# Optimization experiments

Hardware: AMD Instinct MI355X
Metric: run time of the kernel (lower is better)

The kernel has to match this reference:

```python
import jax, jax.numpy as jnp
import numpy as np

N, L, S, D, K, H, G = 512, 1024, 3, 128, 4, 32, 64


def setup_inputs() -> dict:
    key = jax.random.key(0)
    ks = jax.random.split(key, 12)
    f = lambda i, shape, s=1.0: jax.random.normal(ks[i], shape, dtype=jnp.float32) * s
    return dict(
        scores=f(0, (N, 1, L, S)),
        veh_repr=f(1, (N, 1, D)),
        cust_repr=f(2, (N, L, D)),
        edge_emb=f(3, (N, 1, L, D)),
        expert_w1=f(4, (K, S, H), 0.3),
        expert_b1=jnp.zeros((K, H), jnp.float32),
        expert_w2=f(5, (K, H, 1), 0.3),
        expert_b2=jnp.zeros((K, 1), jnp.float32),
        sit_w1=f(6, (2 * D, G), 0.05),
        sit_b1=jnp.zeros((G,), jnp.float32),
        sit_w2=f(7, (G, K), 0.1),
        sit_b2=jnp.zeros((K,), jnp.float32),
        cand_w=f(8, (S, K), 0.3),
        cand_b=jnp.zeros((K,), jnp.float32),
        edge_w=f(9, (D, K), 0.05),
        gate_balance=jnp.zeros((), jnp.float32),
    )


def reference(scores, veh_repr, cust_repr, edge_emb,
              expert_w1, expert_b1, expert_w2, expert_b2,
              sit_w1, sit_b1, sit_w2, sit_b2,
              cand_w, cand_b, edge_w, gate_balance):
    # Inference mode: no gate noise, no dropout (identity at eval).
    # Situation gating: vehicle repr + graph context -> (N,1,K) logits
    graph_ctx = cust_repr.mean(axis=1, keepdims=True)              # (N,1,D)
    sit_in = jnp.concatenate([veh_repr, graph_ctx], axis=-1)       # (N,1,2D)
    hg = jax.nn.gelu(sit_in @ sit_w1 + sit_b1, approximate=False)  # (N,1,G)
    sit_logits = hg @ sit_w2 + sit_b2                              # (N,1,K)

    # Candidate-level gating from raw scores + edge embeddings
    cand_logits = scores @ cand_w + cand_b + edge_emb @ edge_w     # (N,1,L,K)

    alpha = jax.nn.sigmoid(gate_balance)
    gate_logits = alpha * sit_logits[:, :, None, :] + (1.0 - alpha) * cand_logits
    gate_w = jax.nn.softmax(gate_logits, axis=-1)                  # (N,1,L,K)

    # Per-expert tiny MLP over the S score channels
    h = jax.nn.gelu(jnp.einsum('nqls,ksh->nqlkh', scores, expert_w1) + expert_b1,
                    approximate=False)                             # (N,1,L,K,H)
    expert_out = jnp.einsum('nqlkh,kho->nqlko', h, expert_w2)[..., 0] + expert_b2[:, 0]

    fused = (gate_w * expert_out).sum(axis=-1)                     # (N,1,L)
    return fused
```

## Files before the change

kernel.cpp:

```cpp
#include <hip/hip_runtime.h>

#define NN 512
#define LL 1024
#define SS 3
#define DD 128
#define KK 4
#define HH 32
#define GG 64

#define SWZ1  0x041F
#define SWZ2  0x081F
#define SWZ4  0x101F
#define SWZ8  0x201F
#define SWZ16 0x401F
template <int IMM>
__device__ __forceinline__ float swz(float x) {
    return __int_as_float(__builtin_amdgcn_ds_swizzle(__float_as_int(x), IMM));
}

__device__ __forceinline__ float fast_gelu(float x) {
    const float c0 = 0.7978845608028654f;
    const float c1 = 0.7978845608028654f * 0.044715f;
    float u = x * x;
    float y = x * fmaf(c1, u, c0);
    float e = __expf(2.0f * y);
    float r = __builtin_amdgcn_rcpf(e + 1.0f);
    float t = fmaf(-2.0f, r, 1.0f);
    return 0.5f * x * (1.0f + t);
}

__global__ __launch_bounds__(512, 4) void k_all(
    const float* __restrict__ scores, const float* __restrict__ veh,
    const float* __restrict__ cust, const float* __restrict__ edge,
    const float* __restrict__ ew1, const float* __restrict__ eb1,
    const float* __restrict__ ew2, const float* __restrict__ eb2,
    const float* __restrict__ sw1, const float* __restrict__ sb1,
    const float* __restrict__ sw2, const float* __restrict__ sb2,
    const float* __restrict__ cand_w, const float* __restrict__ cand_b,
    const float* __restrict__ edge_w, const float* __restrict__ gbp,
    float* __restrict__ out)
{
    __shared__ float4 red[512];
    __shared__ float sin_[2 * DD];
    __shared__ float hg[GG];
    __shared__ float slds[KK];

    const int n = blockIdx.x;
    const int t = threadIdx.x;
    const int lane = t & 63;
    const int r = lane & 31;

    const int ko = r & 3;
    const int jg = r >> 2;
    const bool kb0 = (r & 1) != 0;
    const bool kb1 = (r & 2) != 0;

    const float4* ew4 = (const float4*)edge_w;
    const float4 wqa = ew4[4 * r + 0];
    const float4 wqb = ew4[4 * r + 1];
    const float4 wqc = ew4[4 * r + 2];
    const float4 wqd = ew4[4 * r + 3];
    const float cw0 = cand_w[0 * KK + ko];
    const float cw1 = cand_w[1 * KK + ko];
    const float cw2 = cand_w[2 * KK + ko];
    const float cb  = cand_b[ko];
    const float4* w1f = (const float4*)ew1;
    const float4 w1a = w1f[(ko * SS + 0) * (HH / 4) + jg];
    const float4 w1b = w1f[(ko * SS + 1) * (HH / 4) + jg];
    const float4 w1c = w1f[(ko * SS + 2) * (HH / 4) + jg];
    const float4 b1v = ((const float4*)eb1)[ko * (HH / 4) + jg];
    const float4 w2v = ((const float4*)ew2)[ko * (HH / 4) + jg];
    const float b2o8 = 0.125f * eb2[ko];
    const float gbv = gbp[0];
    const float alpha = 1.0f / (1.0f + __expf(-gbv));
    const float onema = 1.0f - alpha;

    const int c = t & 31;
    const int rs = t >> 5;
    const float4* cp = (const float4*)(cust + (size_t)n * LL * DD);
    float4 a0 = make_float4(0.f, 0.f, 0.f, 0.f), a1 = a0, a2 = a0, a3 = a0;
    #pragma unroll 4
    for (int i = 0; i < 16; ++i) {
        float4 v0 = cp[(rs + 16 * i      ) * 32 + c];
        float4 v1 = cp[(rs + 16 * i + 256) * 32 + c];
        float4 v2 = cp[(rs + 16 * i + 512) * 32 + c];
        float4 v3 = cp[(rs + 16 * i + 768) * 32 + c];
        a0.x += v0.x; a0.y += v0.y; a0.z += v0.z; a0.w += v0.w;
        a1.x += v1.x; a1.y += v1.y; a1.z += v1.z; a1.w += v1.w;
        a2.x += v2.x; a2.y += v2.y; a2.z += v2.z; a2.w += v2.w;
        a3.x += v3.x; a3.y += v3.y; a3.z += v3.z; a3.w += v3.w;
    }
    a0.x += a1.x + a2.x + a3.x;
    a0.y += a1.y + a2.y + a3.y;
    a0.z += a1.z + a2.z + a3.z;
    a0.w += a1.w + a2.w + a3.w;
    red[t] = a0;
    __syncthreads();

    if (t < 32) {
        float4 s = red[t];
        #pragma unroll
        for (int i = 1; i < 16; i++) {
            float4 v = red[i * 32 + t];
            s.x += v.x; s.y += v.y; s.z += v.z; s.w += v.w;
        }
        const float inv = 1.0f / (float)LL;
        sin_[DD + 4 * t + 0] = s.x * inv;
        sin_[DD + 4 * t + 1] = s.y * inv;
        sin_[DD + 4 * t + 2] = s.z * inv;
        sin_[DD + 4 * t + 3] = s.w * inv;
        float4 vv = ((const float4*)(veh + (size_t)n * DD))[t];
        sin_[4 * t + 0] = vv.x; sin_[4 * t + 1] = vv.y;
        sin_[4 * t + 2] = vv.z; sin_[4 * t + 3] = vv.w;
    }
    __syncthreads();

    if (t < GG) {
        float a = sb1[t];
        #pragma unroll 8
        for (int i = 0; i < 2 * DD; i++)
            a = fmaf(sin_[i], sw1[i * GG + t], a);
        hg[t] = fast_gelu(a);
    }
    __syncthreads();
    if (t < KK) {
        float a = sb2[t];
        #pragma unroll
        for (int g = 0; g < GG; g++)
            a = fmaf(hg[g], sw2[g * KK + t], a);
        slds[t] = a;
    }
    __syncthreads();

    const float sl0 = slds[0], sl1 = slds[1], sl2 = slds[2], sl3 = slds[3];
    float sa_ = kb0 ? sl1 : sl0;
    float sb_ = kb0 ? sl3 : sl2;
    float so  = kb1 ? sb_ : sa_;
    const float sbase = fmaf(alpha, so, onema * cb);

    const int base_el = t >> 5;
    const float* sc_base = scores + (size_t)n * LL * SS;
    const float* ed_base = edge + (size_t)n * LL * DD;
    float* out_base = out + (size_t)n * LL;

    for (int i = 0; i < 16; ++i) {
        const int e0 = base_el + i * 64;
        float4 ev[4];
        float s0[4], s1[4], s2[4];
        #pragma unroll
        for (int u = 0; u < 4; ++u)
            ev[u] = *(const float4*)(ed_base + (size_t)(e0 + u * 16) * DD + r * 4);
        #pragma unroll
        for (int u = 0; u < 4; ++u) {
            const int el = e0 + u * 16;
            s0[u] = sc_base[el * 3 + 0];
            s1[u] = sc_base[el * 3 + 1];
            s2[u] = sc_base[el * 3 + 2];
        }

        float p0[4], p1[4], p2[4], p3[4];
        #pragma unroll
        for (int u = 0; u < 4; ++u) {
            p0[u] = fmaf(ev[u].x, wqa.x, fmaf(ev[u].y, wqb.x, fmaf(ev[u].z, wqc.x, ev[u].w * wqd.x)));
            p1[u] = fmaf(ev[u].x, wqa.y, fmaf(ev[u].y, wqb.y, fmaf(ev[u].z, wqc.y, ev[u].w * wqd.y)));
            p2[u] = fmaf(ev[u].x, wqa.z, fmaf(ev[u].y, wqb.z, fmaf(ev[u].z, wqc.z, ev[u].w * wqd.z)));
            p3[u] = fmaf(ev[u].x, wqa.w, fmaf(ev[u].y, wqb.w, fmaf(ev[u].z, wqc.w, ev[u].w * wqd.w)));
        }
        float P0[4], P2[4];
        #pragma unroll
        for (int u = 0; u < 4; ++u) {
            float g0 = kb0 ? p0[u] : p1[u];
            float g2 = kb0 ? p2[u] : p3[u];
            float k0 = kb0 ? p1[u] : p0[u];
            float k2 = kb0 ? p3[u] : p2[u];
            P0[u] = k0 + swz<SWZ1>(g0);
            P2[u] = k2 + swz<SWZ1>(g2);
        }
        float q[4];
        #pragma unroll
        for (int u = 0; u < 4; ++u) {
            float gv = kb1 ? P0[u] : P2[u];
            float kv = kb1 ? P2[u] : P0[u];
            q[u] = kv + swz<SWZ2>(gv);
        }
        #pragma unroll
        for (int u = 0; u < 4; ++u) q[u] += swz<SWZ4>(q[u]);
        #pragma unroll
        for (int u = 0; u < 4; ++u) q[u] += swz<SWZ8>(q[u]);
        #pragma unroll
        for (int u = 0; u < 4; ++u) q[u] += swz<SWZ16>(q[u]);

        float ex[4];
        #pragma unroll
        for (int u = 0; u < 4; ++u) {
            float sdot = fmaf(s0[u], cw0, fmaf(s1[u], cw1, s2[u] * cw2));
            float gl = fmaf(onema, sdot + q[u], sbase);
            ex[u] = __expf(gl);
        }
        float se[4];
        #pragma unroll
        for (int u = 0; u < 4; ++u) se[u] = ex[u] + swz<SWZ1>(ex[u]);
        #pragma unroll
        for (int u = 0; u < 4; ++u) se[u] += swz<SWZ2>(se[u]);

        float tk[4];
        #pragma unroll
        for (int u = 0; u < 4; ++u) {
            float gw = ex[u] * __builtin_amdgcn_rcpf(se[u]);
            float z, h, acc;
            z = fmaf(s0[u], w1a.x, fmaf(s1[u], w1b.x, fmaf(s2[u], w1c.x, b1v.x))); h = fast_gelu(z); acc = h * w2v.x;
            z = fmaf(s0[u], w1a.y, fmaf(s1[u], w1b.y, fmaf(s2[u], w1c.y, b1v.y))); h = fast_gelu(z); acc = fmaf(h, w2v.y, acc);
            z = fmaf(s0[u], w1a.z, fmaf(s1[u], w1b.z, fmaf(s2[u], w1c.z, b1v.z))); h = fast_gelu(z); acc = fmaf(h, w2v.z, acc);
            z = fmaf(s0[u], w1a.w, fmaf(s1[u], w1b.w, fmaf(s2[u], w1c.w, b1v.w))); h = fast_gelu(z); acc = fmaf(h, w2v.w, acc);
            tk[u] = gw * (acc + b2o8);
        }
        #pragma unroll
        for (int u = 0; u < 4; ++u) tk[u] += swz<SWZ1>(tk[u]);
        #pragma unroll
        for (int u = 0; u < 4; ++u) tk[u] += swz<SWZ2>(tk[u]);
        #pragma unroll
        for (int u = 0; u < 4; ++u) tk[u] += swz<SWZ4>(tk[u]);
        #pragma unroll
        for (int u = 0; u < 4; ++u) tk[u] += swz<SWZ8>(tk[u]);
        #pragma unroll
        for (int u = 0; u < 4; ++u) tk[u] += swz<SWZ16>(tk[u]);

        if (r == 0) {
            #pragma unroll
            for (int u = 0; u < 4; ++u)
                out_base[e0 + u * 16] = tk[u];
        }
    }
}

extern "C" void kernel_launch(void* const* d_in, const int* in_sizes, int n_in,
                              void* d_out, int out_size, void* d_ws, size_t ws_size,
                              hipStream_t stream)
{
    const float* scores = (const float*)d_in[0];
    const float* veh    = (const float*)d_in[1];
    const float* cust   = (const float*)d_in[2];
    const float* edge   = (const float*)d_in[3];
    const float* ew1    = (const float*)d_in[4];
    const float* eb1    = (const float*)d_in[5];
    const float* ew2    = (const float*)d_in[6];
    const float* eb2    = (const float*)d_in[7];
    const float* sw1    = (const float*)d_in[8];
    const float* sb1    = (const float*)d_in[9];
    const float* sw2    = (const float*)d_in[10];
    const float* sb2    = (const float*)d_in[11];
    const float* cw     = (const float*)d_in[12];
    const float* cb     = (const float*)d_in[13];
    const float* egw    = (const float*)d_in[14];
    const float* gb     = (const float*)d_in[15];
    float* out = (float*)d_out;

    hipLaunchKernelGGL(k_all, dim3(NN), dim3(512), 0, stream,
                       scores, veh, cust, edge, ew1, eb1, ew2, eb2,
                       sw1, sb1, sw2, sb2, cw, cb, egw, gb, out);
}
```

Before: 559.9 us.

## Use DPP for lane shuffles, stage scores in LDS, split gating matvec

Replaces the ds_swizzle cross-lane ops within 16-lane groups with DPP quad-permute and row-rotate modifiers, which run in the VALU and avoid an LDS-path round trip. Only the 16-lane swap stays on ds_swizzle. The per-row scores slab is preloaded into LDS with coalesced float4 loads, replacing strided scalar global reads in the main loop. The 256x64 situation matvec is split across 256 threads and then reduced. This adds 12KB of LDS per block, which may lower occupancy at 4 blocks per CU.

```diff
diff --git a/kernel.cpp b/kernel.cpp
--- a/kernel.cpp
+++ b/kernel.cpp
@@ -8,14 +8,19 @@
 #define HH 32
 #define GG 64
 
-#define SWZ1  0x041F
-#define SWZ2  0x081F
-#define SWZ4  0x101F
-#define SWZ8  0x201F
+#define DPP_XOR1 0xB1
+#define DPP_XOR2 0x4E
+#define DPP_ROR4 0x124
+#define DPP_ROR8 0x128
 #define SWZ16 0x401F
-template <int IMM>
-__device__ __forceinline__ float swz(float x) {
-    return __int_as_float(__builtin_amdgcn_ds_swizzle(__float_as_int(x), IMM));
+
+template <int CTRL>
+__device__ __forceinline__ float dppf(float x) {
+    return __int_as_float(__builtin_amdgcn_update_dpp(
+        0, __float_as_int(x), CTRL, 0xF, 0xF, true));
+}
+__device__ __forceinline__ float swz16f(float x) {
+    return __int_as_float(__builtin_amdgcn_ds_swizzle(__float_as_int(x), SWZ16));
 }
 
 __device__ __forceinline__ float fast_gelu(float x) {
@@ -44,6 +49,7 @@
     __shared__ float sin_[2 * DD];
     __shared__ float hg[GG];
     __shared__ float slds[KK];
+    __shared__ float4 sc4[(LL * SS) / 4];
 
     const int n = blockIdx.x;
     const int t = threadIdx.x;
@@ -54,6 +60,12 @@
     const int jg = r >> 2;
     const bool kb0 = (r & 1) != 0;
     const bool kb1 = (r & 2) != 0;
+
+    {
+        const float4* sp4 = (const float4*)(scores + (size_t)n * LL * SS);
+        sc4[t] = sp4[t];
+        if (t < 256) sc4[512 + t] = sp4[512 + t];
+    }
 
     const float4* ew4 = (const float4*)edge_w;
     const float4 wqa = ew4[4 * r + 0];
@@ -115,11 +127,21 @@
     }
     __syncthreads();
 
+    float* redf = (float*)red;
+    if (t < 256) {
+        const int g = t & 63;
+        const int part = t >> 6;
+        float a = 0.f;
+        #pragma unroll 8
+        for (int i = 0; i < 64; ++i) {
+            const int row = part * 64 + i;
+            a = fmaf(sin_[row], sw1[row * GG + g], a);
+        }
+        redf[t] = a;
+    }
+    __syncthreads();
     if (t < GG) {
-        float a = sb1[t];
-        #pragma unroll 8
-        for (int i = 0; i < 2 * DD; i++)
-            a = fmaf(sin_[i], sw1[i * GG + t], a);
+        float a = sb1[t] + redf[t] + redf[t + 64] + redf[t + 128] + redf[t + 192];
         hg[t] = fast_gelu(a);
     }
     __syncthreads();
@@ -139,7 +161,7 @@
     const float sbase = fmaf(alpha, so, onema * cb);
 
     const int base_el = t >> 5;
-    const float* sc_base = scores + (size_t)n * LL * SS;
+    const float* sc_lds = (const float*)sc4;
     const float* ed_base = edge + (size_t)n * LL * DD;
     float* out_base = out + (size_t)n * LL;
 
@@ -153,9 +175,9 @@
         #pragma unroll
         for (int u = 0; u < 4; ++u) {
             const int el = e0 + u * 16;
-            s0[u] = sc_base[el * 3 + 0];
-            s1[u] = sc_base[el * 3 + 1];
-            s2[u] = sc_base[el * 3 + 2];
+            s0[u] = sc_lds[el * 3 + 0];
+            s1[u] = sc_lds[el * 3 + 1];
+            s2[u] = sc_lds[el * 3 + 2];
         }
 
         float p0[4], p1[4], p2[4], p3[4];
@@ -173,22 +195,22 @@
             float g2 = kb0 ? p2[u] : p3[u];
             float k0 = kb0 ? p1[u] : p0[u];
             float k2 = kb0 ? p3[u] : p2[u];
-            P0[u] = k0 + swz<SWZ1>(g0);
-            P2[u] = k2 + swz<SWZ1>(g2);
+            P0[u] = k0 + dppf<DPP_XOR1>(g0);
+            P2[u] = k2 + dppf<DPP_XOR1>(g2);
         }
         float q[4];
         #pragma unroll
         for (int u = 0; u < 4; ++u) {
             float gv = kb1 ? P0[u] : P2[u];
             float kv = kb1 ? P2[u] : P0[u];
-            q[u] = kv + swz<SWZ2>(gv);
-        }
-        #pragma unroll
-        for (int u = 0; u < 4; ++u) q[u] += swz<SWZ4>(q[u]);
-        #pragma unroll
-        for (int u = 0; u < 4; ++u) q[u] += swz<SWZ8>(q[u]);
-        #pragma unroll
-        for (int u = 0; u < 4; ++u) q[u] += swz<SWZ16>(q[u]);
+            q[u] = kv + dppf<DPP_XOR2>(gv);
+        }
+        #pragma unroll
+        for (int u = 0; u < 4; ++u) q[u] += dppf<DPP_ROR4>(q[u]);
+        #pragma unroll
+        for (int u = 0; u < 4; ++u) q[u] += dppf<DPP_ROR8>(q[u]);
+        #pragma unroll
+        for (int u = 0; u < 4; ++u) q[u] += swz16f(q[u]);
 
         float ex[4];
         #pragma unroll
@@ -199,9 +221,9 @@
         }
         float se[4];
         #pragma unroll
-        for (int u = 0; u < 4; ++u) se[u] = ex[u] + swz<SWZ1>(ex[u]);
-        #pragma unroll
-        for (int u = 0; u < 4; ++u) se[u] += swz<SWZ2>(se[u]);
+        for (int u = 0; u < 4; ++u) se[u] = ex[u] + dppf<DPP_XOR1>(ex[u]);
+        #pragma unroll
+        for (int u = 0; u < 4; ++u) se[u] += dppf<DPP_XOR2>(se[u]);
 
         float tk[4];
         #pragma unroll
@@ -215,15 +237,15 @@
             tk[u] = gw * (acc + b2o8);
         }
         #pragma unroll
-        for (int u = 0; u < 4; ++u) tk[u] += swz<SWZ1>(tk[u]);
-        #pragma unroll
-        for (int u = 0; u < 4; ++u) tk[u] += swz<SWZ2>(tk[u]);
-        #pragma unroll
-        for (int u = 0; u < 4; ++u) tk[u] += swz<SWZ4>(tk[u]);
-        #pragma unroll
-        for (int u = 0; u < 4; ++u) tk[u] += swz<SWZ8>(tk[u]);
-        #pragma unroll
-        for (int u = 0; u < 4; ++u) tk[u] += swz<SWZ16>(tk[u]);
+        for (int u = 0; u < 4; ++u) tk[u] += dppf<DPP_XOR1>(tk[u]);
+        #pragma unroll
+        for (int u = 0; u < 4; ++u) tk[u] += dppf<DPP_XOR2>(tk[u]);
+        #pragma unroll
+        for (int u = 0; u < 4; ++u) tk[u] += dppf<DPP_ROR4>(tk[u]);
+        #pragma unroll
+        for (int u = 0; u < 4; ++u) tk[u] += dppf<DPP_ROR8>(tk[u]);
+        #pragma unroll
+        for (int u = 0; u < 4; ++u) tk[u] += swz16f(tk[u]);
 
         if (r == 0) {
             #pragma unroll
```

Measured after the change: 552.9 us. No clear change (-1.2%).
